# Kernel optimization log

Measured on AMD Instinct MI355X. Metric: run time of the kernel, lower is better.

Reference implementation:

```python
import jax, jax.numpy as jnp
import numpy as np

N, E, IN_FEATS, D, H, DIST_DIM, NBOUND = 10000, 160000, 128, 64, 4, 32, 31

def setup_inputs() -> dict:
    key = jax.random.key(0)
    ks = jax.random.split(key, 16)
    gain = 5.0 / 3.0  # tanh gain
    def xavier(k, shape):
        # xavier_normal over the last two dims (fan_in, fan_out) as torch does per-slice
        fan_in, fan_out = shape[-2], shape[-1]
        std = gain * np.sqrt(2.0 / (fan_in + fan_out))
        return jax.random.normal(k, shape, dtype=jnp.float32) * std
    inp = {
        'feat': jax.random.normal(ks[0], (N, IN_FEATS), dtype=jnp.float32),
        'locations': jax.random.normal(ks[1], (N, 3), dtype=jnp.float32),
        'src': jax.random.randint(ks[2], (E,), 0, N),
        'dst': jax.random.randint(ks[3], (E,), 0, N),
        'inter_ids': jax.random.randint(ks[4], (E, H), 0, N),
        'W_fc': xavier(ks[5], (IN_FEATS, H * D)),
        'embed_table': jax.random.normal(ks[6], (NBOUND + 1, DIST_DIM), dtype=jnp.float32),
        'G': xavier(ks[7], (H, DIST_DIM, D)),
        'attn_fc1': xavier(ks[8], (H, 2 * D, D)),
        'attn_fc2': xavier(ks[9], (H, 2 * D, D)),
        'attn_fc3': xavier(ks[10], (H, 2 * D, D)),
        'attn_fc': xavier(ks[11], (H, 3 * D, D)),
        'attn_out': xavier(ks[12], (H, D, 1)),
        'boundaries': jnp.linspace(0.1, 3.1, NBOUND).astype(jnp.float32),
    }
    return inp


def reference(feat, locations, W_fc, embed_table, G, attn_fc1, attn_fc2, attn_fc3,
              attn_fc, attn_out, boundaries, src, dst, inter_ids):
    n = feat.shape[0]
    h = (feat @ W_fc).reshape(n, H, D)                      # [N,H,D]
    pos = locations                                          # [N,3]
    src_pos = pos[src]                                       # [E,3]
    dst_pos = pos[dst]                                       # [E,3]
    inter_pos = pos[inter_ids]                               # [E,H,3]
    h_src = h[src]                                           # [E,H,D]
    h_dst = h[dst]                                           # [E,H,D]
    head_idx = jnp.arange(H)[None, :]
    inter_h = h[inter_ids, head_idx, :]                      # [E,H,D] per-head gather

    e_count = src.shape[0]
    dist1 = jnp.broadcast_to(jnp.linalg.norm(dst_pos - src_pos, axis=-1)[:, None], (e_count, H))
    dist2 = jnp.linalg.norm(dst_pos[:, None, :] - inter_pos, axis=-1)   # [E,H]
    dist_ = jnp.linalg.norm(src_pos[:, None, :] - inter_pos, axis=-1)   # [E,H]

    def dist_embed(dist):
        idx = jnp.searchsorted(boundaries, dist, side='left')  # torch.bucketize(right=False)
        e = embed_table[idx]                                   # [E,H,DIST_DIM]
        return jnp.einsum('ehk,hkd->ehd', e, G)                # [E,H,D]

    de1 = dist_embed(dist1)
    de2 = dist_embed(dist2)
    de_ = dist_embed(dist_)

    d1 = jnp.einsum('ehk,hkd->ehd', jnp.concatenate([h_src, de1], axis=-1), attn_fc1)
    d2 = jnp.einsum('ehk,hkd->ehd', jnp.concatenate([inter_h, de2], axis=-1), attn_fc2)
    d3 = jnp.einsum('ehk,hkd->ehd', jnp.concatenate([h_dst, de_], axis=-1), attn_fc3)

    h_c = jnp.tanh(jnp.einsum('ehk,hkd->ehd', jnp.concatenate([d1, d2, d3], axis=-1), attn_fc))
    e_score = jnp.einsum('ehd,hdo->eho', h_c, attn_out)[..., 0]        # [E,H]

    # edge softmax grouped by destination node
    m = jax.ops.segment_max(e_score, dst, num_segments=n)              # [N,H]
    ex = jnp.exp(e_score - m[dst])
    den = jax.ops.segment_sum(ex, dst, num_segments=n)                 # [N,H]
    a = ex / den[dst]                                                  # [E,H]

    ft = jax.ops.segment_sum(a[:, :, None] * h_src, dst, num_segments=n)  # [N,H,D]
    rst = jnp.mean(ft, axis=1)                                          # merge='mean' -> [N,D]
    return rst
```

## Files before the change

kernel.cpp:

```cpp
#include <hip/hip_runtime.h>
#include <hip/hip_fp16.h>
#include <math.h>

#define N_NODES 10000
#define E_EDGES 160000
#define DMODEL 64
#define H 4
#define NBOUND 31
#define SLOTS 64
#define QREC 1024

typedef _Float16 half8 __attribute__((ext_vector_type(8)));
typedef float floatx4 __attribute__((ext_vector_type(4)));

__device__ __forceinline__ void mm4(const float* __restrict__ S, int aoff,
                                    int astride, int boff, int i0, int j,
                                    int Kdim, float o[4]) {
  float a0 = 0.f, a1 = 0.f, a2 = 0.f, a3 = 0.f;
  for (int t4 = 0; t4 < (Kdim >> 2); ++t4) {
    float4 f0 = *(const float4*)&S[aoff + (i0 + 0) * astride + t4 * 4];
    float4 f1 = *(const float4*)&S[aoff + (i0 + 1) * astride + t4 * 4];
    float4 f2 = *(const float4*)&S[aoff + (i0 + 2) * astride + t4 * 4];
    float4 f3 = *(const float4*)&S[aoff + (i0 + 3) * astride + t4 * 4];
    float b0 = S[boff + (t4 * 4 + 0) * 64 + j];
    float b1 = S[boff + (t4 * 4 + 1) * 64 + j];
    float b2 = S[boff + (t4 * 4 + 2) * 64 + j];
    float b3 = S[boff + (t4 * 4 + 3) * 64 + j];
    a0 += f0.x * b0 + f0.y * b1 + f0.z * b2 + f0.w * b3;
    a1 += f1.x * b0 + f1.y * b1 + f1.z * b2 + f1.w * b3;
    a2 += f2.x * b0 + f2.y * b1 + f2.z * b2 + f2.w * b3;
    a3 += f3.x * b0 + f3.y * b1 + f3.z * b2 + f3.w * b3;
  }
  o[0] = a0; o[1] = a1; o[2] = a2; o[3] = a3;
}

__device__ __forceinline__ int didx(const float* __restrict__ bnd2, float d) {
  int g = (int)(d * 10.0f);
  g = (g < 0) ? 0 : ((g > 31) ? 31 : g);
  g += (bnd2[g + 1] < d) ? 1 : 0;
  g -= (bnd2[g] >= d) ? 1 : 0;
  return g;
}

__global__ __launch_bounds__(256) void prep_kernel(
    const float* __restrict__ fc1, const float* __restrict__ fc2,
    const float* __restrict__ fc3, const float* __restrict__ fcc,
    const float* __restrict__ Wfc, const float* __restrict__ G,
    const float* __restrict__ emb, const float* __restrict__ feat,
    const float* __restrict__ pos, const int* __restrict__ src,
    const int* __restrict__ dst, const int* __restrict__ inter,
    const float* __restrict__ boundaries, __half* __restrict__ bigWT,
    __half* __restrict__ U16, __half* __restrict__ feat16,
    int* __restrict__ widx) {
  __shared__ __align__(16) float S[12288];
  int bi = blockIdx.x;
  int tid = threadIdx.x;
  if (bi >= 1262) {
    if (tid < NBOUND) S[tid + 1] = boundaries[tid];
    if (tid == NBOUND) { S[0] = -INFINITY; S[32] = INFINITY; }
    __syncthreads();
    #pragma unroll
    for (int rep = 0; rep < 2; ++rep) {
      int g = (bi - 1262) * 512 + rep * 256 + tid;
      int e = g >> 2;
      int s = src[e], t = dst[e];
      int it = inter[g];
      float sx = pos[s * 3], sy = pos[s * 3 + 1], sz = pos[s * 3 + 2];
      float tx = pos[t * 3], ty = pos[t * 3 + 1], tz = pos[t * 3 + 2];
      float ix = pos[it * 3], iy = pos[it * 3 + 1], iz = pos[it * 3 + 2];
      float dx = tx - sx, dy = ty - sy, dz = tz - sz;
      float dist1 = sqrtf(dx * dx + dy * dy + dz * dz);
      float ax = tx - ix, ay = ty - iy, az = tz - iz;
      float dist2 = sqrtf(ax * ax + ay * ay + az * az);
      float bx = sx - ix, by = sy - iy, bz = sz - iz;
      float dist_ = sqrtf(bx * bx + by * by + bz * bz);
      int idx1 = didx(S, dist1);
      int idx2 = didx(S, dist2);
      int idx_ = didx(S, dist_);
      widx[g] = idx1 | (idx2 << 5) | (idx_ << 10);
    }
    return;
  }
  if (bi >= 12) {
    int t = (bi - 12) * 256 + tid;
    float4 v = *(const float4*)(feat + t * 4);
    union { uint2 u; __half2 h[2]; } st;
    st.h[0] = __floats2half2_rn(v.x, v.y);
    st.h[1] = __floats2half2_rn(v.z, v.w);
    *(uint2*)&feat16[t * 4] = st.u;
    return;
  }
  int k = bi >> 2, h = bi & 3;
  const float* fck = (k == 0) ? fc1 : (k == 1) ? fc2 : fc3;
  fck += h * 128 * 64;
  const float* F = fcc + h * 192 * 64 + k * 64 * 64;
  int j = tid & 63, ig = tid >> 6;
  float o[4];
  #pragma unroll
  for (int u = 0; u < 4; ++u) {
    ((float4*)S)[u * 256 + tid] = ((const float4*)F)[u * 256 + tid];
    ((float4*)(S + 4096))[u * 256 + tid] = ((const float4*)fck)[u * 256 + tid];
  }
  __syncthreads();
  #pragma unroll
  for (int rg = 0; rg < 4; ++rg) {
    int i0 = ig * 16 + rg * 4;
    mm4(S, 4096, 64, 0, i0, j, 64, o);
    S[8192 + (i0 + 0) * 64 + j] = o[0];
    S[8192 + (i0 + 1) * 64 + j] = o[1];
    S[8192 + (i0 + 2) * 64 + j] = o[2];
    S[8192 + (i0 + 3) * 64 + j] = o[3];
  }
  __syncthreads();
  #pragma unroll
  for (int u = 0; u < 4; ++u) {
    int fi = u * 256 + tid;
    int i = fi >> 4, c4 = fi & 15;
    ((float4*)(S + 4096))[fi] = ((const float4*)(Wfc + i * 256 + h * 64))[c4];
  }
  __syncthreads();
  if (k == 0) {
    #pragma unroll
    for (int u = 0; u < 16; ++u) {
      int idx = u * 256 + tid;
      int i = idx >> 6, jj = idx & 63;
      bigWT[(h * 64 + jj) * 128 + i] = __float2half(S[4096 + idx]);
    }
  }
  #pragma unroll
  for (int rg = 0; rg < 4; ++rg) {
    int i0 = ig * 16 + rg * 4;
    mm4(S, 4096, 64, 8192, i0, j, 64, o);
    int rb = ((k + 1) * 256 + h * 64 + j) * 128;
    bigWT[rb + i0 + 0] = __float2half(o[0]);
    bigWT[rb + i0 + 1] = __float2half(o[1]);
    bigWT[rb + i0 + 2] = __float2half(o[2]);
    bigWT[rb + i0 + 3] = __float2half(o[3]);
  }
  __syncthreads();
  #pragma unroll
  for (int u = 0; u < 4; ++u) {
    int fi = u * 256 + tid;
    int i = fi >> 4, c4 = fi & 15;
    ((float4*)(S + 4096))[fi] =
        ((const float4*)(Wfc + (64 + i) * 256 + h * 64))[c4];
  }
  __syncthreads();
  if (k == 0) {
    #pragma unroll
    for (int u = 0; u < 16; ++u) {
      int idx = u * 256 + tid;
      int i = idx >> 6, jj = idx & 63;
      bigWT[(h * 64 + jj) * 128 + 64 + i] = __float2half(S[4096 + idx]);
    }
  }
  #pragma unroll
  for (int rg = 0; rg < 4; ++rg) {
    int i0 = ig * 16 + rg * 4;
    mm4(S, 4096, 64, 8192, i0, j, 64, o);
    int rb = ((k + 1) * 256 + h * 64 + j) * 128;
    bigWT[rb + 64 + i0 + 0] = __float2half(o[0]);
    bigWT[rb + 64 + i0 + 1] = __float2half(o[1]);
    bigWT[rb + 64 + i0 + 2] = __float2half(o[2]);
    bigWT[rb + 64 + i0 + 3] = __float2half(o[3]);
  }
  __syncthreads();
  #pragma unroll
  for (int u = 0; u < 4; ++u)
    ((float4*)(S + 4096))[u * 256 + tid] =
        ((const float4*)(fck + 4096))[u * 256 + tid];
  __syncthreads();
  #pragma unroll
  for (int rg = 0; rg < 4; ++rg) {
    int i0 = ig * 16 + rg * 4;
    mm4(S, 4096, 64, 0, i0, j, 64, o);
    S[8192 + (i0 + 0) * 64 + j] = o[0];
    S[8192 + (i0 + 1) * 64 + j] = o[1];
    S[8192 + (i0 + 2) * 64 + j] = o[2];
    S[8192 + (i0 + 3) * 64 + j] = o[3];
  }
  __syncthreads();
  #pragma unroll
  for (int u = 0; u < 2; ++u)
    ((float4*)S)[u * 256 + tid] = ((const float4*)(G + h * 2048))[u * 256 + tid];
  ((float4*)(S + 2048))[tid] = ((const float4*)emb)[tid];
  __syncthreads();
  #pragma unroll
  for (int rg = 0; rg < 2; ++rg) {
    int i0 = ig * 8 + rg * 4;
    mm4(S, 0, 64, 8192, i0, j, 64, o);
    S[3072 + (i0 + 0) * 64 + j] = o[0];
    S[3072 + (i0 + 1) * 64 + j] = o[1];
    S[3072 + (i0 + 2) * 64 + j] = o[2];
    S[3072 + (i0 + 3) * 64 + j] = o[3];
  }
  __syncthreads();
  #pragma unroll
  for (int rg = 0; rg < 2; ++rg) {
    int i0 = ig * 8 + rg * 4;
    mm4(S, 2048, 32, 3072, i0, j, 32, o);
    int base = k * 8192 + h * 2048;
    U16[base + (i0 + 0) * 64 + j] = __float2half(o[0]);
    U16[base + (i0 + 1) * 64 + j] = __float2half(o[1]);
    U16[base + (i0 + 2) * 64 + j] = __float2half(o[2]);
    U16[base + (i0 + 3) * 64 + j] = __float2half(o[3]);
  }
}

#define EROW 264

__global__ __launch_bounds__(256) void gemm_init_kernel(
    const __half* __restrict__ feat16, const __half* __restrict__ bigWT,
    __half* __restrict__ qall, int* __restrict__ cursor) {
  __shared__ __align__(16) __half Esm[4][16][EROW];
  int bi = blockIdx.x;
  int tid = threadIdx.x;
  if (bi >= 628) {
    int n = (bi - 628) * 256 + tid;
    if (n < N_NODES) cursor[n] = n * SLOTS;
    return;
  }
  int bx = bi % 157, by = bi / 157;
  int wv = tid >> 6, l = tid & 63;
  int m0 = bx * 64 + wv * 16;
  int n0 = by * 256;
  int lm = l & 15, lk = (l >> 4) * 8;
  int arow = m0 + lm;
  if (arow >= N_NODES) arow = N_NODES - 1;
  const _Float16* fp = (const _Float16*)feat16 + arow * 128 + lk;
  const _Float16* bp = (const _Float16*)bigWT + lk;
  half8 a[4];
  #pragma unroll
  for (int kt = 0; kt < 4; ++kt) a[kt] = *(const half8*)(fp + kt * 32);
  #pragma unroll
  for (int nt = 0; nt < 16; ++nt) {
    floatx4 acc = (floatx4){0.f, 0.f, 0.f, 0.f};
    #pragma unroll
    for (int kt = 0; kt < 4; ++kt) {
      half8 b = *(const half8*)(bp + (n0 + nt * 16 + lm) * 128 + kt * 32);
      acc = __builtin_amdgcn_mfma_f32_16x16x32_f16(a[kt], b, acc, 0, 0, 0);
    }
    int dd = nt * 16 + lm;
    int o = (by == 0) ? ((dd & 63) * 4 + (dd >> 6)) : dd;
    #pragma unroll
    for (int r4 = 0; r4 < 4; ++r4)
      Esm[wv][(l >> 4) * 4 + r4][o] = __float2half(acc[r4]);
  }
  __syncthreads();
  int row = l >> 2;
  int j0 = (l & 3) * 64;
  int m = m0 + row;
  if (m < N_NODES) {
    #pragma unroll
    for (int u = 0; u < 8; ++u) {
      uint4 v = *(const uint4*)&Esm[wv][row][j0 + u * 8];
      *(uint4*)&qall[m * QREC + by * 256 + j0 + u * 8] = v;
    }
  }
}

__device__ __forceinline__ float dpp_row_sum16(float v) {
  int x;
  x = __builtin_amdgcn_update_dpp(0, __float_as_int(v), 0x128, 0xf, 0xf, true);
  v += __int_as_float(x);
  x = __builtin_amdgcn_update_dpp(0, __float_as_int(v), 0x124, 0xf, 0xf, true);
  v += __int_as_float(x);
  x = __builtin_amdgcn_update_dpp(0, __float_as_int(v), 0x122, 0xf, 0xf, true);
  v += __int_as_float(x);
  x = __builtin_amdgcn_update_dpp(0, __float_as_int(v), 0x121, 0xf, 0xf, true);
  v += __int_as_float(x);
  return v;
}

union H4u { uint2 u; __half2 h[2]; };

__device__ __forceinline__ float tanh_dot(H4u A, H4u B, H4u C, H4u X, H4u Y,
                                          H4u Z, float4 a4) {
  __half2 z0 = __hadd2(__hadd2(A.h[0], B.h[0]), __hadd2(C.h[0], X.h[0]));
  z0 = __hadd2(z0, __hadd2(Y.h[0], Z.h[0]));
  __half2 z1 = __hadd2(__hadd2(A.h[1], B.h[1]), __hadd2(C.h[1], X.h[1]));
  z1 = __hadd2(z1, __hadd2(Y.h[1], Z.h[1]));
  float2 f0 = __half22float2(z0);
  float2 f1 = __half22float2(z1);
  const float K = 2.885390082f;
  float p0 = __builtin_amdgcn_exp2f(f0.x * K);
  float p1 = __builtin_amdgcn_exp2f(f0.y * K);
  float p2 = __builtin_amdgcn_exp2f(f1.x * K);
  float p3 = __builtin_amdgcn_exp2f(f1.y * K);
  float r0 = __builtin_amdgcn_rcpf(p0 + 1.0f);
  float r1 = __builtin_amdgcn_rcpf(p1 + 1.0f);
  float r2 = __builtin_amdgcn_rcpf(p2 + 1.0f);
  float r3 = __builtin_amdgcn_rcpf(p3 + 1.0f);
  float dot = a4.x * r0;
  dot = fmaf(a4.y, r1, dot);
  dot = fmaf(a4.z, r2, dot);
  dot = fmaf(a4.w, r3, dot);
  float asum = (a4.x + a4.y) + (a4.z + a4.w);
  return fmaf(-2.0f, dot, asum);
}

__global__ __launch_bounds__(256) void score_fill_kernel(
    const int* __restrict__ src, const int* __restrict__ dst,
    const int* __restrict__ inter, const int* __restrict__ widx,
    const __half* __restrict__ qall, const __half* __restrict__ U16,
    const float* __restrict__ aout, int* __restrict__ cursor,
    float* __restrict__ exsc, int* __restrict__ esrc) {
  int tid = threadIdx.x;
  int wv = tid >> 6, lane = tid & 63;
  int h = lane >> 4, c = lane & 15;
  int e0 = blockIdx.x * 16 + wv * 4;
  int s_[4], t_[4], it_[4], wp_[4];
  #pragma unroll
  for (int q = 0; q < 4; ++q) {
    int e = e0 + q;
    s_[q] = src[e];
    t_[q] = dst[e];
    it_[q] = inter[e * 4 + h];
    wp_[q] = widx[e * 4 + h];
  }
  H4u A[4], B[4], C[4], X[4], Y[4], Z[4];
  #pragma unroll
  for (int q = 0; q < 4; ++q) {
    A[q].u = *(const uint2*)(qall + s_[q] * QREC + 256 + h * 64 + c * 4);
    B[q].u = *(const uint2*)(qall + it_[q] * QREC + 512 + h * 64 + c * 4);
    C[q].u = *(const uint2*)(qall + t_[q] * QREC + 768 + h * 64 + c * 4);
    int i1 = wp_[q] & 31, i2 = (wp_[q] >> 5) & 31, i3 = (wp_[q] >> 10) & 31;
    X[q].u = *(const uint2*)(U16 + (h * 32 + i1) * 64 + c * 4);
    Y[q].u = *(const uint2*)(U16 + 8192 + (h * 32 + i2) * 64 + c * 4);
    Z[q].u = *(const uint2*)(U16 + 16384 + (h * 32 + i3) * 64 + c * 4);
  }
  const float4 a4 = *((const float4*)(aout + h * 64) + c);
  float v[4];
  #pragma unroll
  for (int q = 0; q < 4; ++q)
    v[q] = tanh_dot(A[q], B[q], C[q], X[q], Y[q], Z[q], a4);
  #pragma unroll
  for (int q = 0; q < 4; ++q) v[q] = dpp_row_sum16(v[q]);
  int p[4] = {0, 0, 0, 0};
  if (lane == 0) {
    #pragma unroll
    for (int q = 0; q < 4; ++q) p[q] = atomicAdd(&cursor[t_[q]], 1);
  }
  #pragma unroll
  for (int q = 0; q < 4; ++q) p[q] = __shfl(p[q], 0);
  if (c == 0) {
    #pragma unroll
    for (int q = 0; q < 4; ++q) exsc[p[q] * 4 + h] = __expf(v[q]);
  }
  if (lane == 0) {
    #pragma unroll
    for (int q = 0; q < 4; ++q) esrc[p[q]] = s_[q];
  }
}

__device__ __forceinline__ float4 h4_to_f4(uint2 u) {
  union { uint2 ui; __half2 h[2]; } cc;
  cc.ui = u;
  float2 a = __half22float2(cc.h[0]);
  float2 b = __half22float2(cc.h[1]);
  return make_float4(a.x, a.y, b.x, b.y);
}

__global__ __launch_bounds__(256) void agg_kernel(
    const int* __restrict__ cursor, const int* __restrict__ esrc,
    const float* __restrict__ exsc, const __half* __restrict__ qall,
    float* __restrict__ out) {
  __shared__ float4 sm_num[4][64];
  __shared__ float4 sm_den[4];
  int tid = threadIdx.x;
  int w = tid >> 6, lane = tid & 63;
  int n = blockIdx.x;
  int b = n * SLOTS, e_end = cursor[n];
  float4 num = make_float4(0.f, 0.f, 0.f, 0.f);
  float4 den = make_float4(0.f, 0.f, 0.f, 0.f);
  int i = b + w;
  while (i < e_end) {
    float4 ex[4];
    uint2 hr[4];
    #pragma unroll
    for (int u = 0; u < 4; ++u) {
      ex[u] = make_float4(0.f, 0.f, 0.f, 0.f);
      hr[u] = make_uint2(0, 0);
      int idx = i + u * 4;
      if (idx < e_end) {
        ex[u] = *(const float4*)(exsc + idx * 4);
        hr[u] = *(const uint2*)(qall + esrc[idx] * QREC + lane * 4);
      }
    }
    #pragma unroll
    for (int u = 0; u < 4; ++u) {
      float4 hv = h4_to_f4(hr[u]);
      num.x += ex[u].x * hv.x;
      num.y += ex[u].y * hv.y;
      num.z += ex[u].z * hv.z;
      num.w += ex[u].w * hv.w;
      den.x += ex[u].x; den.y += ex[u].y; den.z += ex[u].z; den.w += ex[u].w;
    }
    i += 16;
  }
  sm_num[w][lane] = num;
  if (lane == 0) sm_den[w] = den;
  __syncthreads();
  if (tid < 64) {
    float4 n0 = sm_num[0][tid], n1 = sm_num[1][tid];
    float4 n2 = sm_num[2][tid], n3 = sm_num[3][tid];
    float4 d0 = sm_den[0], d1 = sm_den[1], d2 = sm_den[2], d3 = sm_den[3];
    float4 ns = make_float4(n0.x + n1.x + n2.x + n3.x, n0.y + n1.y + n2.y + n3.y,
                            n0.z + n1.z + n2.z + n3.z, n0.w + n1.w + n2.w + n3.w);
    float4 ds = make_float4(d0.x + d1.x + d2.x + d3.x, d0.y + d1.y + d2.y + d3.y,
                            d0.z + d1.z + d2.z + d3.z, d0.w + d1.w + d2.w + d3.w);
    float r = 0.f;
    if (e_end > b)
      r = 0.25f * (ns.x / ds.x + ns.y / ds.y + ns.z / ds.z + ns.w / ds.w);
    out[n * 64 + tid] = r;
  }
}

extern "C" void kernel_launch(void* const* d_in, const int* in_sizes, int n_in,
                              void* d_out, int out_size, void* d_ws,
                              size_t ws_size, hipStream_t stream) {
  const float* feat = (const float*)d_in[0];
  const float* loc = (const float*)d_in[1];
  const int* src = (const int*)d_in[2];
  const int* dst = (const int*)d_in[3];
  const int* inter = (const int*)d_in[4];
  const float* Wfc = (const float*)d_in[5];
  const float* emb = (const float*)d_in[6];
  const float* G = (const float*)d_in[7];
  const float* fc1 = (const float*)d_in[8];
  const float* fc2 = (const float*)d_in[9];
  const float* fc3 = (const float*)d_in[10];
  const float* fcc = (const float*)d_in[11];
  const float* aout = (const float*)d_in[12];
  const float* bnd = (const float*)d_in[13];
  float* out = (float*)d_out;

  __half* qall = (__half*)d_ws;
  __half* bigWT = qall + N_NODES * QREC;
  __half* U16 = bigWT + 1024 * 128;
  __half* feat16 = U16 + 3 * H * 2048;
  float* exsc = (float*)(feat16 + N_NODES * 128);
  int* widx = (int*)(exsc + N_NODES * SLOTS * 4);
  int* cursor = widx + E_EDGES * 4;
  int* esrc = cursor + N_NODES;

  prep_kernel<<<2512, 256, 0, stream>>>(fc1, fc2, fc3, fcc, Wfc, G, emb, feat,
                                        loc, src, dst, inter, bnd, bigWT, U16,
                                        feat16, widx);
  gemm_init_kernel<<<668, 256, 0, stream>>>(feat16, bigWT, qall, cursor);
  score_fill_kernel<<<E_EDGES / 16, 256, 0, stream>>>(
      src, dst, inter, widx, qall, U16, aout, cursor, exsc, esrc);
  agg_kernel<<<N_NODES, 256, 0, stream>>>(cursor, esrc, exsc, qall, out);
}
```

Before: 208.7 us.

## Bucket edges by destination in prep and fuse score computation into aggregation

The prep kernel now computes the distance-bucket indices per edge and scatters a packed 16-byte edge record (source, intermediate ids, bucket indices) into per-destination slots using an atomic counter. The separate score-fill kernel is gone: the aggregation kernel reads its node's records, computes each edge's tanh-attention score, exponentiates it and accumulates in place. The feat-to-fp16 conversion moves into the GEMM A-load. This removes the exsc/esrc/widx round trips and one launch, but adds a memset. Node ids are packed into 16 bits, which only works while N stays below 65536.

```diff
diff --git a/kernel.cpp b/kernel.cpp
--- a/kernel.cpp
+++ b/kernel.cpp
@@ -46,48 +46,48 @@
     const float* __restrict__ fc1, const float* __restrict__ fc2,
     const float* __restrict__ fc3, const float* __restrict__ fcc,
     const float* __restrict__ Wfc, const float* __restrict__ G,
-    const float* __restrict__ emb, const float* __restrict__ feat,
-    const float* __restrict__ pos, const int* __restrict__ src,
-    const int* __restrict__ dst, const int* __restrict__ inter,
-    const float* __restrict__ boundaries, __half* __restrict__ bigWT,
-    __half* __restrict__ U16, __half* __restrict__ feat16,
-    int* __restrict__ widx) {
+    const float* __restrict__ emb, const float* __restrict__ pos,
+    const int* __restrict__ src, const int* __restrict__ dst,
+    const int* __restrict__ inter, const float* __restrict__ boundaries,
+    __half* __restrict__ bigWT, __half* __restrict__ U16,
+    int* __restrict__ cnt, uint4* __restrict__ ebuf) {
   __shared__ __align__(16) float S[12288];
   int bi = blockIdx.x;
   int tid = threadIdx.x;
-  if (bi >= 1262) {
+  if (bi >= 12) {
     if (tid < NBOUND) S[tid + 1] = boundaries[tid];
     if (tid == NBOUND) { S[0] = -INFINITY; S[32] = INFINITY; }
     __syncthreads();
-    #pragma unroll
-    for (int rep = 0; rep < 2; ++rep) {
-      int g = (bi - 1262) * 512 + rep * 256 + tid;
-      int e = g >> 2;
-      int s = src[e], t = dst[e];
-      int it = inter[g];
-      float sx = pos[s * 3], sy = pos[s * 3 + 1], sz = pos[s * 3 + 2];
-      float tx = pos[t * 3], ty = pos[t * 3 + 1], tz = pos[t * 3 + 2];
+    int e = (bi - 12) * 256 + tid;
+    int s = src[e], t = dst[e];
+    int4 iv = *(const int4*)&inter[e * 4];
+    int itarr[4] = {iv.x, iv.y, iv.z, iv.w};
+    float sx = pos[s * 3], sy = pos[s * 3 + 1], sz = pos[s * 3 + 2];
+    float tx = pos[t * 3], ty = pos[t * 3 + 1], tz = pos[t * 3 + 2];
+    float dx = tx - sx, dy = ty - sy, dz = tz - sz;
+    float dist1 = sqrtf(dx * dx + dy * dy + dz * dz);
+    unsigned i1 = (unsigned)didx(S, dist1);
+    unsigned w3 = 0, q20 = 0, q_0 = 0;
+    #pragma unroll
+    for (int h = 0; h < 4; ++h) {
+      int it = itarr[h];
       float ix = pos[it * 3], iy = pos[it * 3 + 1], iz = pos[it * 3 + 2];
-      float dx = tx - sx, dy = ty - sy, dz = tz - sz;
-      float dist1 = sqrtf(dx * dx + dy * dy + dz * dz);
       float ax = tx - ix, ay = ty - iy, az = tz - iz;
       float dist2 = sqrtf(ax * ax + ay * ay + az * az);
       float bx = sx - ix, by = sy - iy, bz = sz - iz;
       float dist_ = sqrtf(bx * bx + by * by + bz * bz);
-      int idx1 = didx(S, dist1);
-      int idx2 = didx(S, dist2);
-      int idx_ = didx(S, dist_);
-      widx[g] = idx1 | (idx2 << 5) | (idx_ << 10);
-    }
-    return;
-  }
-  if (bi >= 12) {
-    int t = (bi - 12) * 256 + tid;
-    float4 v = *(const float4*)(feat + t * 4);
-    union { uint2 u; __half2 h[2]; } st;
-    st.h[0] = __floats2half2_rn(v.x, v.y);
-    st.h[1] = __floats2half2_rn(v.z, v.w);
-    *(uint2*)&feat16[t * 4] = st.u;
+      unsigned idx2 = (unsigned)didx(S, dist2);
+      unsigned idx_ = (unsigned)didx(S, dist_);
+      if (h == 0) { q20 = idx2; q_0 = idx_; }
+      else w3 |= (idx2 | (idx_ << 5)) << ((h - 1) * 10);
+    }
+    uint4 rec;
+    rec.x = (unsigned)s | ((unsigned)itarr[0] << 16);
+    rec.y = (unsigned)itarr[1] | ((unsigned)itarr[2] << 16);
+    rec.z = (unsigned)itarr[3] | (i1 << 16) | (q20 << 21) | (q_0 << 26);
+    rec.w = w3;
+    int p = atomicAdd(&cnt[t], 1);
+    if (p < SLOTS) ebuf[t * SLOTS + p] = rec;
     return;
   }
   int k = bi >> 2, h = bi & 3;
@@ -209,17 +209,12 @@
 
 #define EROW 264
 
-__global__ __launch_bounds__(256) void gemm_init_kernel(
-    const __half* __restrict__ feat16, const __half* __restrict__ bigWT,
-    __half* __restrict__ qall, int* __restrict__ cursor) {
+__global__ __launch_bounds__(256) void gemm_kernel(
+    const float* __restrict__ feat, const __half* __restrict__ bigWT,
+    __half* __restrict__ qall) {
   __shared__ __align__(16) __half Esm[4][16][EROW];
   int bi = blockIdx.x;
   int tid = threadIdx.x;
-  if (bi >= 628) {
-    int n = (bi - 628) * 256 + tid;
-    if (n < N_NODES) cursor[n] = n * SLOTS;
-    return;
-  }
   int bx = bi % 157, by = bi / 157;
   int wv = tid >> 6, l = tid & 63;
   int m0 = bx * 64 + wv * 16;
@@ -227,11 +222,20 @@
   int lm = l & 15, lk = (l >> 4) * 8;
   int arow = m0 + lm;
   if (arow >= N_NODES) arow = N_NODES - 1;
-  const _Float16* fp = (const _Float16*)feat16 + arow * 128 + lk;
+  const float* fp = feat + arow * 128 + lk;
   const _Float16* bp = (const _Float16*)bigWT + lk;
   half8 a[4];
   #pragma unroll
-  for (int kt = 0; kt < 4; ++kt) a[kt] = *(const half8*)(fp + kt * 32);
+  for (int kt = 0; kt < 4; ++kt) {
+    float4 u0 = *(const float4*)(fp + kt * 32);
+    float4 u1 = *(const float4*)(fp + kt * 32 + 4);
+    half8 t;
+    t[0] = (_Float16)u0.x; t[1] = (_Float16)u0.y;
+    t[2] = (_Float16)u0.z; t[3] = (_Float16)u0.w;
+    t[4] = (_Float16)u1.x; t[5] = (_Float16)u1.y;
+    t[6] = (_Float16)u1.z; t[7] = (_Float16)u1.w;
+    a[kt] = t;
+  }
   #pragma unroll
   for (int nt = 0; nt < 16; ++nt) {
     floatx4 acc = (floatx4){0.f, 0.f, 0.f, 0.f};
@@ -299,60 +303,6 @@
   return fmaf(-2.0f, dot, asum);
 }
 
-__global__ __launch_bounds__(256) void score_fill_kernel(
-    const int* __restrict__ src, const int* __restrict__ dst,
-    const int* __restrict__ inter, const int* __restrict__ widx,
-    const __half* __restrict__ qall, const __half* __restrict__ U16,
-    const float* __restrict__ aout, int* __restrict__ cursor,
-    float* __restrict__ exsc, int* __restrict__ esrc) {
-  int tid = threadIdx.x;
-  int wv = tid >> 6, lane = tid & 63;
-  int h = lane >> 4, c = lane & 15;
-  int e0 = blockIdx.x * 16 + wv * 4;
-  int s_[4], t_[4], it_[4], wp_[4];
-  #pragma unroll
-  for (int q = 0; q < 4; ++q) {
-    int e = e0 + q;
-    s_[q] = src[e];
-    t_[q] = dst[e];
-    it_[q] = inter[e * 4 + h];
-    wp_[q] = widx[e * 4 + h];
-  }
-  H4u A[4], B[4], C[4], X[4], Y[4], Z[4];
-  #pragma unroll
-  for (int q = 0; q < 4; ++q) {
-    A[q].u = *(const uint2*)(qall + s_[q] * QREC + 256 + h * 64 + c * 4);
-    B[q].u = *(const uint2*)(qall + it_[q] * QREC + 512 + h * 64 + c * 4);
-    C[q].u = *(const uint2*)(qall + t_[q] * QREC + 768 + h * 64 + c * 4);
-    int i1 = wp_[q] & 31, i2 = (wp_[q] >> 5) & 31, i3 = (wp_[q] >> 10) & 31;
-    X[q].u = *(const uint2*)(U16 + (h * 32 + i1) * 64 + c * 4);
-    Y[q].u = *(const uint2*)(U16 + 8192 + (h * 32 + i2) * 64 + c * 4);
-    Z[q].u = *(const uint2*)(U16 + 16384 + (h * 32 + i3) * 64 + c * 4);
-  }
-  const float4 a4 = *((const float4*)(aout + h * 64) + c);
-  float v[4];
-  #pragma unroll
-  for (int q = 0; q < 4; ++q)
-    v[q] = tanh_dot(A[q], B[q], C[q], X[q], Y[q], Z[q], a4);
-  #pragma unroll
-  for (int q = 0; q < 4; ++q) v[q] = dpp_row_sum16(v[q]);
-  int p[4] = {0, 0, 0, 0};
-  if (lane == 0) {
-    #pragma unroll
-    for (int q = 0; q < 4; ++q) p[q] = atomicAdd(&cursor[t_[q]], 1);
-  }
-  #pragma unroll
-  for (int q = 0; q < 4; ++q) p[q] = __shfl(p[q], 0);
-  if (c == 0) {
-    #pragma unroll
-    for (int q = 0; q < 4; ++q) exsc[p[q] * 4 + h] = __expf(v[q]);
-  }
-  if (lane == 0) {
-    #pragma unroll
-    for (int q = 0; q < 4; ++q) esrc[p[q]] = s_[q];
-  }
-}
-
 __device__ __forceinline__ float4 h4_to_f4(uint2 u) {
   union { uint2 ui; __half2 h[2]; } cc;
   cc.ui = u;
@@ -361,42 +311,62 @@
   return make_float4(a.x, a.y, b.x, b.y);
 }
 
-__global__ __launch_bounds__(256) void agg_kernel(
-    const int* __restrict__ cursor, const int* __restrict__ esrc,
-    const float* __restrict__ exsc, const __half* __restrict__ qall,
-    float* __restrict__ out) {
+__global__ __launch_bounds__(256) void score_agg_kernel(
+    const int* __restrict__ cnt, const uint4* __restrict__ ebuf,
+    const __half* __restrict__ qall, const __half* __restrict__ U16,
+    const float* __restrict__ aout, float* __restrict__ out) {
+  __shared__ uint4 recs[SLOTS];
   __shared__ float4 sm_num[4][64];
   __shared__ float4 sm_den[4];
   int tid = threadIdx.x;
   int w = tid >> 6, lane = tid & 63;
+  int h = lane >> 4, c = lane & 15;
   int n = blockIdx.x;
-  int b = n * SLOTS, e_end = cursor[n];
+  int deg = cnt[n];
+  if (deg > SLOTS) deg = SLOTS;
+  if (tid < deg) recs[tid] = ebuf[n * SLOTS + tid];
+  H4u C;
+  C.u = *(const uint2*)(qall + n * QREC + 768 + h * 64 + c * 4);
+  const float4 a4 = *((const float4*)(aout + h * 64) + c);
+  __syncthreads();
   float4 num = make_float4(0.f, 0.f, 0.f, 0.f);
   float4 den = make_float4(0.f, 0.f, 0.f, 0.f);
-  int i = b + w;
-  while (i < e_end) {
-    float4 ex[4];
-    uint2 hr[4];
-    #pragma unroll
-    for (int u = 0; u < 4; ++u) {
-      ex[u] = make_float4(0.f, 0.f, 0.f, 0.f);
-      hr[u] = make_uint2(0, 0);
-      int idx = i + u * 4;
-      if (idx < e_end) {
-        ex[u] = *(const float4*)(exsc + idx * 4);
-        hr[u] = *(const uint2*)(qall + esrc[idx] * QREC + lane * 4);
-      }
-    }
-    #pragma unroll
-    for (int u = 0; u < 4; ++u) {
-      float4 hv = h4_to_f4(hr[u]);
-      num.x += ex[u].x * hv.x;
-      num.y += ex[u].y * hv.y;
-      num.z += ex[u].z * hv.z;
-      num.w += ex[u].w * hv.w;
-      den.x += ex[u].x; den.y += ex[u].y; den.z += ex[u].z; den.w += ex[u].w;
-    }
-    i += 16;
+  for (int i = w; i < deg; i += 4) {
+    uint4 r = recs[i];
+    int s = r.x & 0xffff;
+    int it = (h == 0) ? (int)(r.x >> 16)
+           : (h == 1) ? (int)(r.y & 0xffff)
+           : (h == 2) ? (int)(r.y >> 16) : (int)(r.z & 0xffff);
+    unsigned i1 = (r.z >> 16) & 31;
+    unsigned q2h, q_h;
+    if (h == 0) {
+      q2h = (r.z >> 21) & 31;
+      q_h = (r.z >> 26) & 31;
+    } else {
+      unsigned f = r.w >> ((h - 1) * 10);
+      q2h = f & 31;
+      q_h = (f >> 5) & 31;
+    }
+    H4u A, B, X, Y, Z;
+    A.u = *(const uint2*)(qall + s * QREC + 256 + h * 64 + c * 4);
+    B.u = *(const uint2*)(qall + it * QREC + 512 + h * 64 + c * 4);
+    X.u = *(const uint2*)(U16 + (h * 32 + i1) * 64 + c * 4);
+    Y.u = *(const uint2*)(U16 + 8192 + (h * 32 + q2h) * 64 + c * 4);
+    Z.u = *(const uint2*)(U16 + 16384 + (h * 32 + q_h) * 64 + c * 4);
+    uint2 hr = *(const uint2*)(qall + s * QREC + lane * 4);
+    float v = tanh_dot(A, B, C, X, Y, Z, a4);
+    v = dpp_row_sum16(v);
+    float ex = __expf(v);
+    float e0 = __shfl(ex, 0);
+    float e1 = __shfl(ex, 16);
+    float e2 = __shfl(ex, 32);
+    float e3 = __shfl(ex, 48);
+    float4 hv = h4_to_f4(hr);
+    num.x += e0 * hv.x;
+    num.y += e1 * hv.y;
+    num.z += e2 * hv.z;
+    num.w += e3 * hv.w;
+    den.x += e0; den.y += e1; den.z += e2; den.w += e3;
   }
   sm_num[w][lane] = num;
   if (lane == 0) sm_den[w] = den;
@@ -410,7 +380,7 @@
     float4 ds = make_float4(d0.x + d1.x + d2.x + d3.x, d0.y + d1.y + d2.y + d3.y,
                             d0.z + d1.z + d2.z + d3.z, d0.w + d1.w + d2.w + d3.w);
     float r = 0.f;
-    if (e_end > b)
+    if (deg > 0)
       r = 0.25f * (ns.x / ds.x + ns.y / ds.y + ns.z / ds.z + ns.w / ds.w);
     out[n * 64 + tid] = r;
   }
@@ -438,17 +408,14 @@
   __half* qall = (__half*)d_ws;
   __half* bigWT = qall + N_NODES * QREC;
   __half* U16 = bigWT + 1024 * 128;
-  __half* feat16 = U16 + 3 * H * 2048;
-  float* exsc = (float*)(feat16 + N_NODES * 128);
-  int* widx = (int*)(exsc + N_NODES * SLOTS * 4);
-  int* cursor = widx + E_EDGES * 4;
-  int* esrc = cursor + N_NODES;
-
-  prep_kernel<<<2512, 256, 0, stream>>>(fc1, fc2, fc3, fcc, Wfc, G, emb, feat,
-                                        loc, src, dst, inter, bnd, bigWT, U16,
-                                        feat16, widx);
-  gemm_init_kernel<<<668, 256, 0, stream>>>(feat16, bigWT, qall, cursor);
-  score_fill_kernel<<<E_EDGES / 16, 256, 0, stream>>>(
-      src, dst, inter, widx, qall, U16, aout, cursor, exsc, esrc);
-  agg_kernel<<<N_NODES, 256, 0, stream>>>(cursor, esrc, exsc, qall, out);
-}
+  uint4* ebuf = (uint4*)(U16 + 3 * H * 2048);
+  int* cnt = (int*)(ebuf + N_NODES * SLOTS);
+
+  hipMemsetAsync(cnt, 0, N_NODES * sizeof(int), stream);
+  prep_kernel<<<12 + E_EDGES / 256, 256, 0, stream>>>(
+      fc1, fc2, fc3, fcc, Wfc, G, emb, loc, src, dst, inter, bnd, bigWT, U16,
+      cnt, ebuf);
+  gemm_kernel<<<628, 256, 0, stream>>>(feat, bigWT, qall);
+  score_agg_kernel<<<N_NODES, 256, 0, stream>>>(cnt, ebuf, qall, U16, aout,
+                                                out);
+}
```

Result: slower. 236.9 us (+13.5%).
